# Performance work log

Hardware: AMD Instinct MI355X
Metric: run time of the kernel (lower is better)

## Reference

```python
import jax, jax.numpy as jnp
import numpy as np

MARGIN = 0.1
SCALE_POS = 2.0
SCALE_NEG = 50.0
THRESH = 0.5
EPS = 1e-5


def setup_inputs() -> dict:
    key = jax.random.key(0)
    k1, k2 = jax.random.split(key)
    feats = jax.random.normal(k1, (4096, 2, 192), dtype=jnp.float32)
    labels = jax.random.randint(k2, (4096,), 0, 4096, dtype=jnp.int64)
    return {"feats": feats, "labels": labels}


def reference(feats, labels):
    B, n_utt, D = feats.shape
    lab = jnp.repeat(labels, n_utt)            # [N]
    f = feats.reshape(-1, D)                   # [N, D]
    N = f.shape[0]

    sim = f @ f.T                              # [N, N]
    # F.normalize(sim): L2-normalize each row, eps=1e-12
    row_norm = jnp.maximum(jnp.linalg.norm(sim, axis=1, keepdims=True), 1e-12)
    S = sim / row_norm

    same = lab[None, :] == lab[:, None]        # [N, N]
    pos_mask = same & (S < 1.0 - EPS)          # pos_pair_ (includes self if < 1-eps)
    neg_mask = ~same                           # neg_pair_

    min_pos = jnp.min(jnp.where(pos_mask, S, jnp.inf), axis=1)    # per-row min(pos_pair_)
    max_neg = jnp.max(jnp.where(neg_mask, S, -jnp.inf), axis=1)   # per-row max(neg_pair_)

    neg_keep = neg_mask & (S > (min_pos - MARGIN)[:, None])
    pos_keep = pos_mask & (S < (max_neg + MARGIN)[:, None])

    has_neg = jnp.any(neg_keep, axis=1)
    has_pos = jnp.any(pos_keep, axis=1)
    valid = has_neg & has_pos

    pos_sum = jnp.sum(jnp.where(pos_keep, jnp.exp(-SCALE_POS * (S - THRESH)), 0.0), axis=1)
    neg_sum = jnp.sum(jnp.where(neg_keep, jnp.exp(SCALE_NEG * (S - THRESH)), 0.0), axis=1)

    row_loss = (1.0 / SCALE_POS) * jnp.log1p(pos_sum) + (1.0 / SCALE_NEG) * jnp.log1p(neg_sum)
    loss = jnp.sum(jnp.where(valid, row_loss, 0.0)) / N

    # prec1 = percent of rows skipped for having no surviving negatives
    prec1 = jnp.sum(~has_neg).astype(jnp.float32) * 100.0 / N
    return loss, prec1
```

## Files before the change

kernel.cpp:

```cpp
#include <hip/hip_runtime.h>
#include <math.h>

typedef float  f32x4  __attribute__((ext_vector_type(4)));
typedef int    int4v  __attribute__((ext_vector_type(4)));
typedef int    int8v  __attribute__((ext_vector_type(8)));

constexpr float MARGIN    = 0.1f;
constexpr float SCALE_POS = 2.0f;
constexpr float SCALE_NEG = 50.0f;
constexpr float THRESH    = 0.5f;
constexpr float ONE_EPS   = 1.0f - 1e-5f;
constexpr float LOG2E     = 1.4426950408889634f;
constexpr float BC        = -(SCALE_NEG * THRESH * LOG2E);
constexpr float VCUT_COEF = (36.0674f - 30.0f) / (SCALE_NEG * LOG2E);

constexpr int D      = 192;
constexpr int KP     = 256;
constexpr int RT     = 4;
constexpr int RPW    = 64;
constexpr int RPB    = 256;
constexpr int CSPLIT = 16;

constexpr int TILE_B8 = 4096;
constexpr int SCALE1  = 0x7f7f7f7f;

__device__ inline float fast_exp2(float x) {
#if __has_builtin(__builtin_amdgcn_exp2f)
  return __builtin_amdgcn_exp2f(x);
#else
  return exp2f(x);
#endif
}

__device__ inline void pin_frag8(int8v& v) {
  asm volatile("" : "+v"(v));
}

__global__ __launch_bounds__(1024) void k_prep(
    const float* __restrict__ f, unsigned char* __restrict__ pk8, int nrows,
    const int* __restrict__ labs, int* __restrict__ hist_g, int* __restrict__ offs_g,
    int* __restrict__ bucket, float* __restrict__ accum, int n)
{
  if (blockIdx.x < 64) {
    int gid = blockIdx.x * 1024 + threadIdx.x;
    int r = gid >> 3, j = gid & 7;
    if (r >= nrows) return;
    float x[32];
    if (j < 6) {
      const float* src = f + (size_t)r * D + j * 32;
#pragma unroll
      for (int i = 0; i < 8; ++i) {
        float4 v = *(const float4*)(src + i * 4);
        x[i * 4 + 0] = v.x; x[i * 4 + 1] = v.y; x[i * 4 + 2] = v.z; x[i * 4 + 3] = v.w;
      }
    } else {
#pragma unroll
      for (int i = 0; i < 32; ++i) x[i] = 0.f;
    }
    union { int s[8]; int8v v; } u;
#pragma unroll
    for (int i = 0; i < 8; ++i) {
      int p = __builtin_amdgcn_cvt_pk_fp8_f32(x[i * 4 + 0], x[i * 4 + 1], 0, false);
      p     = __builtin_amdgcn_cvt_pk_fp8_f32(x[i * 4 + 2], x[i * 4 + 3], p, true);
      u.s[i] = p;
    }
    int tile = r >> 4, c = r & 15, g = j >> 2, qq = j & 3;
    *(int8v*)(pk8 + (size_t)tile * TILE_B8 + g * 2048 + (qq * 16 + c) * 32) = u.v;
    return;
  }

  __shared__ int histL[4096];
  __shared__ int offsL[4096];
  __shared__ int scanb[1024];
  const int t = threadIdx.x;

  if (t < 3) accum[t] = 0.f;
  for (int i = t; i < 4096; i += 1024) histL[i] = 0;
  __syncthreads();
  for (int i = t; i < n; i += 1024) atomicAdd(&histL[labs[i]], 1);
  __syncthreads();
  int base = t * 4;
  int v[4]; int ls = 0;
  for (int k = 0; k < 4; ++k) { v[k] = ls; ls += histL[base + k]; }
  scanb[t] = ls;
  __syncthreads();
  for (int o = 1; o < 1024; o <<= 1) {
    int x = (t >= o) ? scanb[t - o] : 0;
    __syncthreads();
    scanb[t] += x;
    __syncthreads();
  }
  int ebase = scanb[t] - ls;
  for (int k = 0; k < 4; ++k) {
    offsL[base + k] = ebase + v[k];
    offs_g[base + k] = ebase + v[k];
    hist_g[base + k] = histL[base + k];
  }
  __syncthreads();
  for (int i = t; i < 4096; i += 1024) histL[i] = 0;
  __syncthreads();
  for (int i = t; i < n; i += 1024) {
    int lab = labs[i];
    int p = atomicAdd(&histL[lab], 1);
    bucket[offsL[lab] + p] = i;
  }
}

__global__ __launch_bounds__(256, 2) void k_pass1(
    const unsigned char* __restrict__ pk8, const int* __restrict__ labs,
    float* __restrict__ sumsqP, float* __restrict__ maxnegP,
    int N, int cps)
{
  __shared__ int ldsLab[512];

  const int tid  = threadIdx.x;
  const int lane = tid & 63;
  const int w    = tid >> 6;
  const int q    = lane >> 4;
  const int c    = lane & 15;
  const int cs   = blockIdx.x & (CSPLIT - 1);
  const int rbb  = blockIdx.x / CSPLIT;
  const int rowbase = rbb * RPB + w * RPW;
  const int col0 = cs * cps;
  const int ctile0 = col0 >> 4;
  const int ntiles = cps >> 4;

  for (int i = tid; i < cps; i += 256) ldsLab[i] = labs[(col0 + i) >> 1];

  int8v afr[RT][2];
#pragma unroll
  for (int rt = 0; rt < RT; ++rt)
#pragma unroll
    for (int g = 0; g < 2; ++g) {
      afr[rt][g] = *(const int8v*)(pk8 + (size_t)((rowbase >> 4) + rt) * TILE_B8 + g * 2048 + lane * 32);
      pin_frag8(afr[rt][g]);
    }

  int labrow[RT][4];
#pragma unroll
  for (int rt = 0; rt < RT; ++rt)
#pragma unroll
    for (int rr = 0; rr < 4; ++rr)
      labrow[rt][rr] = labs[(rowbase + rt * 16 + q * 4 + rr) >> 1];

  float ssq[RT][4], mxn[RT][4];
#pragma unroll
  for (int rt = 0; rt < RT; ++rt)
#pragma unroll
    for (int rr = 0; rr < 4; ++rr) { ssq[rt][rr] = 0.f; mxn[rt][rr] = -INFINITY; }

  __syncthreads();

  auto loadB = [&](int tile, int8v (&bf)[2]) {
    const unsigned char* bp = pk8 + (size_t)(ctile0 + tile) * TILE_B8 + lane * 32;
#pragma unroll
    for (int g = 0; g < 2; ++g) bf[g] = *(const int8v*)(bp + g * 2048);
  };
  auto compute = [&](const int8v (&bf)[2], int t) {
    const int labcol = ldsLab[t * 16 + c];
    f32x4 acc[RT];
#pragma unroll
    for (int rt = 0; rt < RT; ++rt) acc[rt] = 0.f;
#pragma unroll
    for (int g = 0; g < 2; ++g)
#pragma unroll
      for (int rt = 0; rt < RT; ++rt)
        acc[rt] = __builtin_amdgcn_mfma_scale_f32_16x16x128_f8f6f4(
            afr[rt][g], bf[g], acc[rt], 0, 0, 0, SCALE1, 0, SCALE1);
#pragma unroll
    for (int rt = 0; rt < RT; ++rt)
#pragma unroll
      for (int rr = 0; rr < 4; ++rr) {
        float v = acc[rt][rr];
        ssq[rt][rr] = fmaf(v, v, ssq[rt][rr]);
        float vm = (labrow[rt][rr] == labcol) ? -INFINITY : v;
        mxn[rt][rr] = fmaxf(mxn[rt][rr], vm);
      }
  };

  auto wrap = [&](int x) { return (x < ntiles) ? x : 0; };
  int8v b0[2], b1[2], b2[2], b3[2];
  loadB(0, b0);
  loadB(1, b1);
  for (int t = 0; t < ntiles; t += 4) {
    loadB(wrap(t + 2), b2); compute(b0, t);
    loadB(wrap(t + 3), b3); compute(b1, t + 1);
    loadB(wrap(t + 4), b0); compute(b2, t + 2);
    loadB(wrap(t + 5), b1); compute(b3, t + 3);
  }

#pragma unroll
  for (int rt = 0; rt < RT; ++rt)
#pragma unroll
    for (int rr = 0; rr < 4; ++rr) {
      float s = ssq[rt][rr], m = mxn[rt][rr];
#pragma unroll
      for (int msk = 1; msk < 16; msk <<= 1) {
        s += __shfl_xor(s, msk, 64);
        m = fmaxf(m, __shfl_xor(m, msk, 64));
      }
      if (c == 0) {
        int row = rowbase + rt * 16 + q * 4 + rr;
        sumsqP[(size_t)cs * N + row] = s;
        maxnegP[(size_t)cs * N + row] = m;
      }
    }
}

__global__ void k_rowstats(
    const float* __restrict__ f, const int* __restrict__ labs,
    const float* __restrict__ sumsqP, const float* __restrict__ maxnegP,
    const int* __restrict__ offs, const int* __restrict__ hist, const int* __restrict__ bucket,
    float* __restrict__ nthr2, float* __restrict__ arow,
    float* __restrict__ validf, float* __restrict__ hasnegf, float* __restrict__ posloss,
    int N)
{
  const int lane = threadIdx.x & 63;
  const int row  = blockIdx.x * 4 + (threadIdx.x >> 6);

  float s = 0.f, m = -INFINITY;
  if (lane < CSPLIT) {
    s = sumsqP[(size_t)lane * N + row];
    m = maxnegP[(size_t)lane * N + row];
  }
#pragma unroll
  for (int msk = 1; msk < 64; msk <<= 1) {
    s += __shfl_xor(s, msk, 64);
    m = fmaxf(m, __shfl_xor(m, msk, 64));
  }
  float nrm = fmaxf(sqrtf(s), 1e-12f);
  float inv = 1.0f / nrm;
  float maxnegS = m * inv;
  float posth = fminf(ONE_EPS, maxnegS + MARGIN);

  const int lab = labs[row >> 1];
  const int beg = offs[lab], cnt = hist[lab];
  const float* fi = f + (size_t)row * D;
  float x0 = fi[lane], x1 = fi[lane + 64], x2 = fi[lane + 128];

  float minp = INFINITY, psum = 0.f; int pcnt = 0;
  for (int t = 0; t < cnt; ++t) {
    int smp = bucket[beg + t];
#pragma unroll
    for (int u = 0; u < 2; ++u) {
      const float* fj = f + (size_t)(smp * 2 + u) * D;
      float p = x0 * fj[lane] + x1 * fj[lane + 64] + x2 * fj[lane + 128];
#pragma unroll
      for (int msk = 1; msk < 64; msk <<= 1) p += __shfl_xor(p, msk, 64);
      minp = fminf(minp, p);
      float S = p * inv;
      if (S < posth) {
        psum += fast_exp2((THRESH - S) * (SCALE_POS * LOG2E));
        pcnt++;
      }
    }
  }

  float minS = minp * inv;
  float min_pos = (minS < ONE_EPS) ? minS : INFINITY;
  bool hneg = maxnegS > (min_pos - MARGIN);
  bool valid = hneg && (pcnt > 0);
  if (lane == 0) {
    nthr2[row]   = fmaxf((min_pos - MARGIN) * nrm, VCUT_COEF * nrm);
    arow[row]    = inv * (SCALE_NEG * LOG2E);
    validf[row]  = valid ? 1.f : 0.f;
    hasnegf[row] = hneg ? 1.f : 0.f;
    posloss[row] = valid ? ((1.0f / SCALE_POS) * log1pf(psum)) : 0.f;
  }
}

__global__ __launch_bounds__(256, 2) void k_pass2(
    const unsigned char* __restrict__ pk8,
    const float* __restrict__ nthr2, const float* __restrict__ arow,
    const float* __restrict__ maxnegP,
    float* __restrict__ negsumP, int N, int cps)
{
  const int lane = threadIdx.x & 63;
  const int w    = threadIdx.x >> 6;
  const int q    = lane >> 4;
  const int c    = lane & 15;
  const int cs   = blockIdx.x & (CSPLIT - 1);
  const int rbb  = blockIdx.x / CSPLIT;
  const int rowbase = rbb * RPB + w * RPW;
  const int ctile0 = (cs * cps) >> 4;
  const int ntiles = cps >> 4;

  {
    int myrow = rowbase + lane;
    float mn = maxnegP[(size_t)cs * N + myrow];
    float th = nthr2[myrow];
    unsigned long long bal = __ballot(mn > th);
    if (bal == 0ull) {
      negsumP[(size_t)cs * N + myrow] = 0.f;
      return;
    }
  }

  int8v afr[RT][2];
#pragma unroll
  for (int rt = 0; rt < RT; ++rt)
#pragma unroll
    for (int g = 0; g < 2; ++g) {
      afr[rt][g] = *(const int8v*)(pk8 + (size_t)((rowbase >> 4) + rt) * TILE_B8 + g * 2048 + lane * 32);
      pin_frag8(afr[rt][g]);
    }

  float nthrv[RT][4], arw[RT][4], ns[RT][4];
#pragma unroll
  for (int rt = 0; rt < RT; ++rt)
#pragma unroll
    for (int rr = 0; rr < 4; ++rr) {
      int row = rowbase + rt * 16 + q * 4 + rr;
      nthrv[rt][rr] = nthr2[row];
      arw[rt][rr]   = arow[row];
      ns[rt][rr]    = 0.f;
    }

  auto loadB = [&](int tile, int8v (&bf)[2]) {
    const unsigned char* bp = pk8 + (size_t)(ctile0 + tile) * TILE_B8 + lane * 32;
#pragma unroll
    for (int g = 0; g < 2; ++g) bf[g] = *(const int8v*)(bp + g * 2048);
  };
  auto compute = [&](const int8v (&bf)[2]) {
    f32x4 acc[RT];
#pragma unroll
    for (int rt = 0; rt < RT; ++rt) acc[rt] = 0.f;
#pragma unroll
    for (int g = 0; g < 2; ++g)
#pragma unroll
      for (int rt = 0; rt < RT; ++rt)
        acc[rt] = __builtin_amdgcn_mfma_scale_f32_16x16x128_f8f6f4(
            afr[rt][g], bf[g], acc[rt], 0, 0, 0, SCALE1, 0, SCALE1);
#pragma unroll
    for (int rt = 0; rt < RT; ++rt)
#pragma unroll
      for (int rr = 0; rr < 4; ++rr) {
        float v = acc[rt][rr];
        float e = fast_exp2(fmaf(v, arw[rt][rr], BC));
        ns[rt][rr] += (v > nthrv[rt][rr]) ? e : 0.f;
      }
  };

  int8v b0[2], b1[2];
  loadB(0, b0);
  for (int t = 0; t < ntiles; t += 2) {
    loadB(t + 1, b1);
    compute(b0);
    int nx = t + 2; nx = (nx < ntiles) ? nx : 0;
    loadB(nx, b0);
    compute(b1);
  }

#pragma unroll
  for (int rt = 0; rt < RT; ++rt)
#pragma unroll
    for (int rr = 0; rr < 4; ++rr) {
      float sv = ns[rt][rr];
#pragma unroll
      for (int msk = 1; msk < 16; msk <<= 1) sv += __shfl_xor(sv, msk, 64);
      if (c == 0) {
        int row = rowbase + rt * 16 + q * 4 + rr;
        negsumP[(size_t)cs * N + row] = sv;
      }
    }
}

__global__ void k_final(const float* __restrict__ negsumP, const float* __restrict__ posloss,
                        const float* __restrict__ validf, const float* __restrict__ hasnegf,
                        float* __restrict__ accum, float* __restrict__ out, int N)
{
  int i = blockIdx.x * blockDim.x + threadIdx.x;
  float lacc = 0.f, nacc = 0.f;
  if (i < N) {
    float nsum = 0.f;
    for (int cs2 = 0; cs2 < CSPLIT; ++cs2) nsum += negsumP[(size_t)cs2 * N + i];
    lacc = validf[i] * (posloss[i] + (1.0f / SCALE_NEG) * log1pf(nsum));
    nacc = 1.0f - hasnegf[i];
  }
#pragma unroll
  for (int msk = 1; msk < 64; msk <<= 1) {
    lacc += __shfl_xor(lacc, msk, 64);
    nacc += __shfl_xor(nacc, msk, 64);
  }
  __shared__ float sl[4], sn[4];
  __shared__ bool isLast;
  int wid = threadIdx.x >> 6, lane = threadIdx.x & 63;
  if (lane == 0) { sl[wid] = lacc; sn[wid] = nacc; }
  __syncthreads();
  if (threadIdx.x == 0) {
    float L = sl[0] + sl[1] + sl[2] + sl[3];
    float Nn = sn[0] + sn[1] + sn[2] + sn[3];
    atomicAdd(&accum[0], L);
    atomicAdd(&accum[1], Nn);
    __threadfence();
    int tkt = atomicAdd((int*)&accum[2], 1);
    isLast = (tkt == (int)gridDim.x - 1);
  }
  __syncthreads();
  if (isLast && threadIdx.x == 0) {
    __threadfence();
    out[0] = accum[0] / (float)N;
    out[1] = accum[1] * 100.0f / (float)N;
  }
}

extern "C" void kernel_launch(void* const* d_in, const int* in_sizes, int n_in,
                              void* d_out, int out_size, void* d_ws, size_t ws_size,
                              hipStream_t stream)
{
  (void)n_in; (void)out_size; (void)ws_size;
  const float* f    = (const float*)d_in[0];
  const int*   labs = (const int*)d_in[1];
  const int Bs = in_sizes[1];
  const int N  = 2 * Bs;

  char* ws = (char*)d_ws;
  size_t off = 0;
  auto alloc = [&](size_t bytes) -> void* {
    void* p = ws + off;
    off += (bytes + 255) & ~(size_t)255;
    return p;
  };
  unsigned char* pk8 = (unsigned char*)alloc((size_t)N * KP);
  float* sumsqP  = (float*)alloc((size_t)CSPLIT * N * sizeof(float));
  float* maxnegP = (float*)alloc((size_t)CSPLIT * N * sizeof(float));
  float* negsumP = (float*)alloc((size_t)CSPLIT * N * sizeof(float));
  float* nthr2   = (float*)alloc((size_t)N * sizeof(float));
  float* arow    = (float*)alloc((size_t)N * sizeof(float));
  float* validf  = (float*)alloc((size_t)N * sizeof(float));
  float* hasnegf = (float*)alloc((size_t)N * sizeof(float));
  float* posloss = (float*)alloc((size_t)N * sizeof(float));
  int* hist   = (int*)alloc((size_t)Bs * sizeof(int));
  int* offs   = (int*)alloc((size_t)Bs * sizeof(int));
  int* bucket = (int*)alloc((size_t)Bs * sizeof(int));
  float* accum = (float*)alloc(4 * sizeof(float));

  k_prep<<<65, 1024, 0, stream>>>(f, pk8, N, labs, hist, offs, bucket, accum, Bs);

  const int cps   = N / CSPLIT;
  const int grid1 = (N / RPB) * CSPLIT;
  k_pass1<<<grid1, 256, 0, stream>>>(pk8, labs, sumsqP, maxnegP, N, cps);
  k_rowstats<<<N / 4, 256, 0, stream>>>(f, labs, sumsqP, maxnegP, offs, hist, bucket,
                                        nthr2, arow, validf, hasnegf, posloss, N);
  k_pass2<<<grid1, 256, 0, stream>>>(pk8, nthr2, arow, maxnegP, negsumP, N, cps);
  k_final<<<N / 256, 256, 0, stream>>>(negsumP, posloss, validf, hasnegf, accum, (float*)d_out, N);
}
```

Baseline: 101.1 us.

## Exploit Gram matrix symmetry in pass1 by computing only upper-triangular block pairs

Pass1 now runs over 256x256 block pairs (i<=j) of the symmetric similarity matrix instead of every row-block/column-split, and off-diagonal blocks also produce column-wise sum-of-squares and max-negative partials through LDS. This roughly halves the FP8 MFMA work in the first pass. The cost is extra per-tile column reductions, shuffles and LDS traffic, plus 32 partial slots per row instead of 16. Pass2 merges two slots for its early-exit check, and negsumP now aliases sumsqP.

After: 137.2 us. +35.8%, slower.

```diff
diff --git a/kernel.cpp b/kernel.cpp
--- a/kernel.cpp
+++ b/kernel.cpp
@@ -21,6 +21,11 @@
 constexpr int RPB    = 256;
 constexpr int CSPLIT = 16;
 
+constexpr int NSLOT  = 32;
+constexpr int CBLK   = 256;
+constexpr int NTILES = CBLK / 16;
+constexpr int NPAIR  = (NSLOT * (NSLOT - 1)) / 2;
+
 constexpr int TILE_B8 = 4096;
 constexpr int SCALE1  = 0x7f7f7f7f;
 
@@ -108,24 +113,31 @@
 
 __global__ __launch_bounds__(256, 2) void k_pass1(
     const unsigned char* __restrict__ pk8, const int* __restrict__ labs,
-    float* __restrict__ sumsqP, float* __restrict__ maxnegP,
-    int N, int cps)
-{
-  __shared__ int ldsLab[512];
+    float* __restrict__ sumsqP, float* __restrict__ maxnegP, int N)
+{
+  __shared__ int   ldsLab[CBLK];
+  __shared__ float colS[4][CBLK];
+  __shared__ float colM[4][CBLK];
 
   const int tid  = threadIdx.x;
   const int lane = tid & 63;
   const int w    = tid >> 6;
   const int q    = lane >> 4;
   const int c    = lane & 15;
-  const int cs   = blockIdx.x & (CSPLIT - 1);
-  const int rbb  = blockIdx.x / CSPLIT;
-  const int rowbase = rbb * RPB + w * RPW;
-  const int col0 = cs * cps;
-  const int ctile0 = col0 >> 4;
-  const int ntiles = cps >> 4;
-
-  for (int i = tid; i < cps; i += 256) ldsLab[i] = labs[(col0 + i) >> 1];
+
+  int i, j;
+  if ((int)blockIdx.x < NPAIR) {
+    int t = blockIdx.x; i = 0;
+    while (t >= NSLOT - 1 - i) { t -= NSLOT - 1 - i; ++i; }
+    j = i + 1 + t;
+  } else {
+    i = j = blockIdx.x - NPAIR;
+  }
+  const bool offd = (i != j);
+  const int rowbase = i * CBLK + w * RPW;
+  const int ctile0  = j * NTILES;
+
+  ldsLab[tid] = labs[(j * CBLK + tid) >> 1];
 
   int8v afr[RT][2];
 #pragma unroll
@@ -167,6 +179,7 @@
       for (int rt = 0; rt < RT; ++rt)
         acc[rt] = __builtin_amdgcn_mfma_scale_f32_16x16x128_f8f6f4(
             afr[rt][g], bf[g], acc[rt], 0, 0, 0, SCALE1, 0, SCALE1);
+    float csA = 0.f, cmA = -INFINITY;
 #pragma unroll
     for (int rt = 0; rt < RT; ++rt)
 #pragma unroll
@@ -175,14 +188,23 @@
         ssq[rt][rr] = fmaf(v, v, ssq[rt][rr]);
         float vm = (labrow[rt][rr] == labcol) ? -INFINITY : v;
         mxn[rt][rr] = fmaxf(mxn[rt][rr], vm);
-      }
+        csA = fmaf(v, v, csA);
+        cmA = fmaxf(cmA, vm);
+      }
+    if (offd) {
+      csA += __shfl_xor(csA, 16, 64);
+      csA += __shfl_xor(csA, 32, 64);
+      cmA = fmaxf(cmA, __shfl_xor(cmA, 16, 64));
+      cmA = fmaxf(cmA, __shfl_xor(cmA, 32, 64));
+      if (q == 0) { colS[w][t * 16 + c] = csA; colM[w][t * 16 + c] = cmA; }
+    }
   };
 
-  auto wrap = [&](int x) { return (x < ntiles) ? x : 0; };
+  auto wrap = [&](int x) { return (x < NTILES) ? x : 0; };
   int8v b0[2], b1[2], b2[2], b3[2];
   loadB(0, b0);
   loadB(1, b1);
-  for (int t = 0; t < ntiles; t += 4) {
+  for (int t = 0; t < NTILES; t += 4) {
     loadB(wrap(t + 2), b2); compute(b0, t);
     loadB(wrap(t + 3), b3); compute(b1, t + 1);
     loadB(wrap(t + 4), b0); compute(b2, t + 2);
@@ -201,10 +223,20 @@
       }
       if (c == 0) {
         int row = rowbase + rt * 16 + q * 4 + rr;
-        sumsqP[(size_t)cs * N + row] = s;
-        maxnegP[(size_t)cs * N + row] = m;
-      }
-    }
+        sumsqP[(size_t)j * N + row] = s;
+        maxnegP[(size_t)j * N + row] = m;
+      }
+    }
+
+  if (offd) {
+    __syncthreads();
+    float s4 = colS[0][tid] + colS[1][tid] + colS[2][tid] + colS[3][tid];
+    float m4 = fmaxf(fmaxf(colM[0][tid], colM[1][tid]),
+                     fmaxf(colM[2][tid], colM[3][tid]));
+    const int colrow = j * CBLK + tid;
+    sumsqP[(size_t)i * N + colrow] = s4;
+    maxnegP[(size_t)i * N + colrow] = m4;
+  }
 }
 
 __global__ void k_rowstats(
@@ -219,7 +251,7 @@
   const int row  = blockIdx.x * 4 + (threadIdx.x >> 6);
 
   float s = 0.f, m = -INFINITY;
-  if (lane < CSPLIT) {
+  if (lane < NSLOT) {
     s = sumsqP[(size_t)lane * N + row];
     m = maxnegP[(size_t)lane * N + row];
   }
@@ -287,7 +319,8 @@
 
   {
     int myrow = rowbase + lane;
-    float mn = maxnegP[(size_t)cs * N + myrow];
+    float mn = fmaxf(maxnegP[(size_t)(2 * cs) * N + myrow],
+                     maxnegP[(size_t)(2 * cs + 1) * N + myrow]);
     float th = nthr2[myrow];
     unsigned long long bal = __ballot(mn > th);
     if (bal == 0ull) {
@@ -422,9 +455,9 @@
     return p;
   };
   unsigned char* pk8 = (unsigned char*)alloc((size_t)N * KP);
-  float* sumsqP  = (float*)alloc((size_t)CSPLIT * N * sizeof(float));
-  float* maxnegP = (float*)alloc((size_t)CSPLIT * N * sizeof(float));
-  float* negsumP = (float*)alloc((size_t)CSPLIT * N * sizeof(float));
+  float* sumsqP  = (float*)alloc((size_t)NSLOT * N * sizeof(float));
+  float* maxnegP = (float*)alloc((size_t)NSLOT * N * sizeof(float));
+  float* negsumP = sumsqP;
   float* nthr2   = (float*)alloc((size_t)N * sizeof(float));
   float* arow    = (float*)alloc((size_t)N * sizeof(float));
   float* validf  = (float*)alloc((size_t)N * sizeof(float));
@@ -437,11 +470,11 @@
 
   k_prep<<<65, 1024, 0, stream>>>(f, pk8, N, labs, hist, offs, bucket, accum, Bs);
 
-  const int cps   = N / CSPLIT;
-  const int grid1 = (N / RPB) * CSPLIT;
-  k_pass1<<<grid1, 256, 0, stream>>>(pk8, labs, sumsqP, maxnegP, N, cps);
+  k_pass1<<<NPAIR + NSLOT, 256, 0, stream>>>(pk8, labs, sumsqP, maxnegP, N);
   k_rowstats<<<N / 4, 256, 0, stream>>>(f, labs, sumsqP, maxnegP, offs, hist, bucket,
                                         nthr2, arow, validf, hasnegf, posloss, N);
-  k_pass2<<<grid1, 256, 0, stream>>>(pk8, nthr2, arow, maxnegP, negsumP, N, cps);
+  const int cps   = N / CSPLIT;
+  const int grid2 = (N / RPB) * CSPLIT;
+  k_pass2<<<grid2, 256, 0, stream>>>(pk8, nthr2, arow, maxnegP, negsumP, N, cps);
   k_final<<<N / 256, 256, 0, stream>>>(negsumP, posloss, validf, hasnegf, accum, (float*)d_out, N);
 }
```
